# Performance work log

Hardware: AMD Instinct MI355X
Metric: run time of the kernel (lower is better)

The kernel has to match this reference:

```python
import jax, jax.numpy as jnp
import numpy as np

B, N, IN, H, E, P, L = 32, 5000, 16, 64, 2_560_000, 300, 100


def setup_inputs() -> dict:
    key = jax.random.key(0)
    ks = jax.random.split(key, 10)
    return {
        "h": jax.random.normal(ks[0], (B * N, IN), jnp.float32),
        "src": jax.random.randint(ks[1], (E,), 0, B * N, jnp.int32),
        "dst": jax.random.randint(ks[2], (E,), 0, B * N, jnp.int32),
        "pathway": jax.random.randint(ks[3], (P, L), 0, N, jnp.int32),
        "num_graphs": B,
        "W1": jax.random.normal(ks[4], (IN, H), jnp.float32) / np.float32(np.sqrt(IN)),
        "b1": jnp.zeros((H,), jnp.float32),
        "W2": jax.random.normal(ks[5], (H, H), jnp.float32) / np.float32(np.sqrt(H)),
        "b2": jnp.zeros((H,), jnp.float32),
        "w_lin1": jax.random.normal(ks[6], (2 * H, 1), jnp.float32) / np.float32(np.sqrt(2 * H)),
        "b_lin1": jnp.zeros((1,), jnp.float32),
        "W_out": jax.random.normal(ks[7], (P, 2), jnp.float32) / np.float32(np.sqrt(P)),
        "b_out": jnp.zeros((2,), jnp.float32),
    }


def reference(h, src, dst, pathway, num_graphs, W1, b1, W2, b2, w_lin1, b_lin1, W_out, b_out):
    BN = h.shape[0]
    # GINConv (eps=0, 'sum' aggregation): lin(h + sum_{j in N(i)} h_j), then relu
    agg0 = jax.ops.segment_sum(h[src], dst, num_segments=BN)
    h1 = jax.nn.relu((h + agg0) @ W1 + b1)            # [BN, H]
    agg1 = jax.ops.segment_sum(h1[src], dst, num_segments=BN)
    h2 = jax.nn.relu((h1 + agg1) @ W2 + b2)           # [BN, H]

    Hd = h2.shape[-1]
    hb = h2.reshape(num_graphs, -1, Hd)               # [B, N, H]
    Pn = pathway.shape[0]
    # Faithful to source: mean branch is the WHOLE-graph mean repeated per pathway
    mean_rep = jnp.broadcast_to(hb.mean(axis=1)[:, None, :], (num_graphs, Pn, Hd))
    # Sum-pool over each pathway's node subset
    sum_path = hb[:, pathway, :].sum(axis=2)          # [B, P, H]
    feat = jnp.concatenate([mean_rep, sum_path], axis=-1)  # [B, P, 2H]
    s = jnp.tanh(feat @ w_lin1 + b_lin1)[..., 0]      # [B, P]
    return jax.nn.softmax(s @ W_out + b_out, axis=-1)  # [B, 2]
```

## Files before the change

### kernel.cpp

```cpp
#include <hip/hip_runtime.h>
#include <hip/hip_bf16.h>
#include <math.h>

static inline size_t align256(size_t x) { return (x + 255) & ~size_t(255); }

#define SLOTS 48

__global__ __launch_bounds__(256) void place_shard(const int* __restrict__ src,
                                                   const int* __restrict__ dst,
                                                   int* __restrict__ counts,
                                                   int* __restrict__ esrc_pad, int E, int BN) {
    int s  = blockIdx.x & 7;
    int bs = blockIdx.x >> 3;
    int nb = gridDim.x >> 3;
    int lo = (int)(((long long)BN * s) >> 3);
    int hi = (int)(((long long)BN * (s + 1)) >> 3);
    for (int e = bs * 256 + threadIdx.x; e < E; e += nb * 256) {
        int d = __builtin_nontemporal_load(dst + e);
        if (d >= lo && d < hi) {
            int rank = atomicAdd(&counts[d], 1);
            if (rank < SLOTS)
                esrc_pad[(size_t)d * SLOTS + rank] = __builtin_nontemporal_load(src + e);
        }
    }
}

__global__ __launch_bounds__(256, 8) void gin1_fused(const float* __restrict__ h,
                                                     const int* __restrict__ cnts,
                                                     const int* __restrict__ esrc_pad,
                                                     const float* __restrict__ W1,
                                                     const float* __restrict__ b1,
                                                     __hip_bfloat16* __restrict__ h1, int BN) {
    __shared__ float xb[4][16];
    __shared__ int   ibuf[4][64];
    int tid = threadIdx.x;
    int lane = tid & 63, wv = tid >> 6;
    int fg = lane >> 4, ft = lane & 15;
    int gw = (int)((blockIdx.x * blockDim.x + tid) >> 6);
    int nw = (int)((gridDim.x * blockDim.x) >> 6);
    float wcol[16];
#pragma unroll
    for (int k = 0; k < 16; ++k) wcol[k] = W1[k * 64 + lane];
    float breg = b1[lane];
    for (int i = gw; i < BN; i += nw) {
        float acc = (fg == 0) ? h[(size_t)i * 16 + ft] : 0.f;
        int deg = min(cnts[i], SLOTS);
        if (lane < deg) ibuf[wv][lane] = esrc_pad[(size_t)i * SLOTS + lane];
        int jj = fg;
        for (; jj + 4 < deg; jj += 8) {
            int s0 = ibuf[wv][jj];
            int s1 = ibuf[wv][jj + 4];
            acc += h[(size_t)s0 * 16 + ft] + h[(size_t)s1 * 16 + ft];
        }
        if (jj < deg) acc += h[(size_t)ibuf[wv][jj] * 16 + ft];
        acc += __shfl_xor(acc, 16, 64);
        acc += __shfl_xor(acc, 32, 64);
        if (lane < 16) xb[wv][lane] = acc;
        float o = breg;
#pragma unroll
        for (int k4 = 0; k4 < 4; ++k4) {
            float4 xv = *(const float4*)&xb[wv][k4 * 4];
            o = fmaf(xv.x, wcol[k4 * 4 + 0], o);
            o = fmaf(xv.y, wcol[k4 * 4 + 1], o);
            o = fmaf(xv.z, wcol[k4 * 4 + 2], o);
            o = fmaf(xv.w, wcol[k4 * 4 + 3], o);
        }
        h1[(size_t)i * 64 + lane] = __float2bfloat16(fmaxf(o, 0.f));
    }
}

__global__ __launch_bounds__(256, 8) void gather64_bf16(const __hip_bfloat16* __restrict__ h1,
                                                        const int* __restrict__ cnts,
                                                        const int* __restrict__ esrc_pad,
                                                        __hip_bfloat16* __restrict__ tmp, int BN) {
    __shared__ int ibuf[4][64];
    int tid = threadIdx.x;
    int lane = tid & 63, wv = tid >> 6;
    int gw = (int)((blockIdx.x * blockDim.x + tid) >> 6);
    int nw = (int)((gridDim.x * blockDim.x) >> 6);
    const __hip_bfloat16* hl = h1 + lane;
    for (int i = gw; i < BN; i += nw) {
        float acc = __bfloat162float(hl[(size_t)i * 64]);
        int deg = min(cnts[i], SLOTS);
        if (lane < deg) ibuf[wv][lane] = esrc_pad[(size_t)i * SLOTS + lane];
        int jj = 0;
        for (; jj + 16 <= deg; jj += 16) {
            int4 ia = *(const int4*)&ibuf[wv][jj];
            int4 ib = *(const int4*)&ibuf[wv][jj + 4];
            int4 ic = *(const int4*)&ibuf[wv][jj + 8];
            int4 id = *(const int4*)&ibuf[wv][jj + 12];
            float v0 = __bfloat162float(hl[(size_t)ia.x * 64]);
            float v1 = __bfloat162float(hl[(size_t)ia.y * 64]);
            float v2 = __bfloat162float(hl[(size_t)ia.z * 64]);
            float v3 = __bfloat162float(hl[(size_t)ia.w * 64]);
            float v4 = __bfloat162float(hl[(size_t)ib.x * 64]);
            float v5 = __bfloat162float(hl[(size_t)ib.y * 64]);
            float v6 = __bfloat162float(hl[(size_t)ib.z * 64]);
            float v7 = __bfloat162float(hl[(size_t)ib.w * 64]);
            float v8 = __bfloat162float(hl[(size_t)ic.x * 64]);
            float v9 = __bfloat162float(hl[(size_t)ic.y * 64]);
            float va = __bfloat162float(hl[(size_t)ic.z * 64]);
            float vb = __bfloat162float(hl[(size_t)ic.w * 64]);
            float vc = __bfloat162float(hl[(size_t)id.x * 64]);
            float vd = __bfloat162float(hl[(size_t)id.y * 64]);
            float ve = __bfloat162float(hl[(size_t)id.z * 64]);
            float vf = __bfloat162float(hl[(size_t)id.w * 64]);
            acc += (((v0 + v1) + (v2 + v3)) + ((v4 + v5) + (v6 + v7)))
                 + (((v8 + v9) + (va + vb)) + ((vc + vd) + (ve + vf)));
        }
        for (; jj + 8 <= deg; jj += 8) {
            int4 ia = *(const int4*)&ibuf[wv][jj];
            int4 ib = *(const int4*)&ibuf[wv][jj + 4];
            float v0 = __bfloat162float(hl[(size_t)ia.x * 64]);
            float v1 = __bfloat162float(hl[(size_t)ia.y * 64]);
            float v2 = __bfloat162float(hl[(size_t)ia.z * 64]);
            float v3 = __bfloat162float(hl[(size_t)ia.w * 64]);
            float v4 = __bfloat162float(hl[(size_t)ib.x * 64]);
            float v5 = __bfloat162float(hl[(size_t)ib.y * 64]);
            float v6 = __bfloat162float(hl[(size_t)ib.z * 64]);
            float v7 = __bfloat162float(hl[(size_t)ib.w * 64]);
            acc += ((v0 + v1) + (v2 + v3)) + ((v4 + v5) + (v6 + v7));
        }
        for (; jj + 4 <= deg; jj += 4) {
            int4 ia = *(const int4*)&ibuf[wv][jj];
            float v0 = __bfloat162float(hl[(size_t)ia.x * 64]);
            float v1 = __bfloat162float(hl[(size_t)ia.y * 64]);
            float v2 = __bfloat162float(hl[(size_t)ia.z * 64]);
            float v3 = __bfloat162float(hl[(size_t)ia.w * 64]);
            acc += (v0 + v1) + (v2 + v3);
        }
        for (; jj < deg; ++jj) acc += __bfloat162float(hl[(size_t)ibuf[wv][jj] * 64]);
        tmp[(size_t)i * 64 + lane] = __float2bfloat16(acc);
    }
}

__global__ __launch_bounds__(256, 4) void lin2_qr(const __hip_bfloat16* __restrict__ tmp,
                                                  const float* __restrict__ W2,
                                                  const float* __restrict__ b2,
                                                  const float* __restrict__ wlin,
                                                  float* __restrict__ q,
                                                  float* __restrict__ r, int BN) {
    __shared__ float xbuf[4][64];
    int tid = threadIdx.x;
    int lane = tid & 63, wv = tid >> 6;
    int gw = (int)((blockIdx.x * blockDim.x + tid) >> 6);
    int nw = (int)((gridDim.x * blockDim.x) >> 6);
    float wcol[64];
#pragma unroll
    for (int k = 0; k < 64; ++k) wcol[k] = W2[k * 64 + lane];
    float breg = b2[lane];
    float wlo = wlin[lane];
    float whi = wlin[64 + lane];
    for (int i = gw; i < BN; i += nw) {
        xbuf[wv][lane] = __bfloat162float(tmp[(size_t)i * 64 + lane]);
        float outv = breg;
#pragma unroll
        for (int k4 = 0; k4 < 16; ++k4) {
            float4 xv = *(const float4*)&xbuf[wv][k4 * 4];
            outv = fmaf(xv.x, wcol[k4 * 4 + 0], outv);
            outv = fmaf(xv.y, wcol[k4 * 4 + 1], outv);
            outv = fmaf(xv.z, wcol[k4 * 4 + 2], outv);
            outv = fmaf(xv.w, wcol[k4 * 4 + 3], outv);
        }
        float h2v = fmaxf(outv, 0.f);
        float qv = h2v * whi;
        float rv = h2v * wlo;
#pragma unroll
        for (int off = 32; off >= 1; off >>= 1) {
            qv += __shfl_xor(qv, off, 64);
            rv += __shfl_xor(rv, off, 64);
        }
        if (lane == 0) {
            q[i] = qv;
            r[i] = rv;
        }
    }
}


__global__ __launch_bounds__(256) void reduce_m2(const float* __restrict__ r,
                                                 float* __restrict__ m2, int N, int bpg) {
    int b = blockIdx.x / bpg, sub = blockIdx.x % bpg;
    const float* rb = r + (size_t)b * N;
    float a = 0.f;
    for (int n = sub * 256 + threadIdx.x; n < N; n += bpg * 256) a += rb[n];
    __shared__ float red[256];
    red[threadIdx.x] = a;
    __syncthreads();
    for (int off = 128; off >= 1; off >>= 1) {
        if (threadIdx.x < off) red[threadIdx.x] += red[threadIdx.x + off];
        __syncthreads();
    }
    if (threadIdx.x == 0) unsafeAtomicAdd(&m2[b], red[0]);
}

__global__ __launch_bounds__(256) void pathway_score_wave(const float* __restrict__ q,
                                                          const int* __restrict__ pathway,
                                                          const float* __restrict__ m2,
                                                          const float* __restrict__ blin,
                                                          float* __restrict__ s,
                                                          int N, int P, int L, float invN,
                                                          int B) {
    int wid = (int)((blockIdx.x * blockDim.x + threadIdx.x) >> 6);
    int lane = threadIdx.x & 63;
    if (wid >= B * P) return;
    int b = wid / P, p = wid % P;
    const int* pw = pathway + (size_t)p * L;
    const float* qb = q + (size_t)b * N;
    float sum = 0.f;
    for (int l = lane; l < L; l += 64) sum += qb[pw[l]];
#pragma unroll
    for (int off = 32; off >= 1; off >>= 1) sum += __shfl_xor(sum, off, 64);
    if (lane == 0) s[wid] = tanhf(sum + m2[b] * invN + blin[0]);
}

__global__ __launch_bounds__(64) void out_softmax_wave(const float* __restrict__ s,
                                                       const float* __restrict__ Wout,
                                                       const float* __restrict__ bout,
                                                       float* __restrict__ out, int P) {
    int b = blockIdx.x;
    int lane = threadIdx.x;
    const float* sb = s + (size_t)b * P;
    float a0 = 0.f, a1 = 0.f;
    for (int p = lane; p < P; p += 64) {
        float sv = sb[p];
        a0 = fmaf(sv, Wout[p * 2 + 0], a0);
        a1 = fmaf(sv, Wout[p * 2 + 1], a1);
    }
#pragma unroll
    for (int off = 32; off >= 1; off >>= 1) {
        a0 += __shfl_xor(a0, off, 64);
        a1 += __shfl_xor(a1, off, 64);
    }
    if (lane == 0) {
        float l0 = a0 + bout[0], l1 = a1 + bout[1];
        float m = fmaxf(l0, l1);
        float e0 = expf(l0 - m), e1 = expf(l1 - m);
        float inv = 1.f / (e0 + e1);
        out[b * 2 + 0] = e0 * inv;
        out[b * 2 + 1] = e1 * inv;
    }
}

extern "C" void kernel_launch(void* const* d_in, const int* in_sizes, int n_in,
                              void* d_out, int out_size, void* d_ws, size_t ws_size,
                              hipStream_t stream) {
    const float* h       = (const float*)d_in[0];
    const int*   src     = (const int*)d_in[1];
    const int*   dst     = (const int*)d_in[2];
    const int*   pathway = (const int*)d_in[3];
    const float* W1      = (const float*)d_in[5];
    const float* b1      = (const float*)d_in[6];
    const float* W2      = (const float*)d_in[7];
    const float* b2      = (const float*)d_in[8];
    const float* wlin    = (const float*)d_in[9];
    const float* blin    = (const float*)d_in[10];
    const float* Wout    = (const float*)d_in[11];
    const float* bout    = (const float*)d_in[12];
    float*       out     = (float*)d_out;

    const int BN = in_sizes[0] / 16;
    const int E  = in_sizes[1];
    const int P  = in_sizes[11] / 2;
    const int L  = in_sizes[3] / P;
    const int B  = out_size / 2;
    const int N  = BN / B;

    char* ws = (char*)d_ws;
    size_t o = 0;
    __hip_bfloat16* h1  = (__hip_bfloat16*)(ws + o); o += align256((size_t)BN * 64 * 2);
    __hip_bfloat16* tmp = (__hip_bfloat16*)(ws + o); o += align256((size_t)BN * 64 * 2);
    float* qbuf     = (float*)(ws + o); o += align256((size_t)BN * 4);
    float* rbuf     = (float*)(ws + o); o += align256((size_t)BN * 4);
    float* m2       = (float*)(ws + o); o += align256((size_t)B * 4);
    float* sbuf     = (float*)(ws + o); o += align256((size_t)B * P * 4);
    int*   counts   = (int*)(ws + o);   o += align256((size_t)BN * 4);
    int*   esrc_pad = (int*)(ws + o);   o += align256((size_t)BN * SLOTS * 4);
    (void)ws_size; (void)n_in;

    hipMemsetAsync(counts, 0, (size_t)BN * 4, stream);
    hipMemsetAsync(m2, 0, (size_t)B * 4, stream);
    place_shard<<<2048, 256, 0, stream>>>(src, dst, counts, esrc_pad, E, BN);

    gin1_fused<<<4096, 256, 0, stream>>>(h, counts, esrc_pad, W1, b1, h1, BN);

    gather64_bf16<<<4096, 256, 0, stream>>>(h1, counts, esrc_pad, tmp, BN);
    lin2_qr<<<2048, 256, 0, stream>>>(tmp, W2, b2, wlin, qbuf, rbuf, BN);

    reduce_m2<<<B * 8, 256, 0, stream>>>(rbuf, m2, N, 8);
    pathway_score_wave<<<(B * P + 3) / 4, 256, 0, stream>>>(qbuf, pathway, m2, blin, sbuf,
                                                            N, P, L, 1.0f / (float)N, B);
    out_softmax_wave<<<B, 64, 0, stream>>>(sbuf, Wout, bout, out, P);
}
```

Before: 289.4 us.

## Drop destination-sharded edge placement and gather layer-1 inputs from bf16 copy

The edge bucketing kernel no longer makes each block scan every edge eight times (once per destination shard). It now processes each edge once with a global atomic, trading lower dst read traffic for less locality in the atomics and scattered writes. Separately, the input features are converted to bf16 in a new pass, so the first GIN gather reads half as many bytes per neighbour row. This adds an extra kernel launch and introduces bf16 rounding into the layer-1 aggregation.

```diff
diff --git a/kernel.cpp b/kernel.cpp
--- a/kernel.cpp
+++ b/kernel.cpp
@@ -6,26 +6,35 @@
 
 #define SLOTS 48
 
-__global__ __launch_bounds__(256) void place_shard(const int* __restrict__ src,
-                                                   const int* __restrict__ dst,
-                                                   int* __restrict__ counts,
-                                                   int* __restrict__ esrc_pad, int E, int BN) {
-    int s  = blockIdx.x & 7;
-    int bs = blockIdx.x >> 3;
-    int nb = gridDim.x >> 3;
-    int lo = (int)(((long long)BN * s) >> 3);
-    int hi = (int)(((long long)BN * (s + 1)) >> 3);
-    for (int e = bs * 256 + threadIdx.x; e < E; e += nb * 256) {
+__global__ __launch_bounds__(256) void place_pad(const int* __restrict__ src,
+                                                 const int* __restrict__ dst,
+                                                 int* __restrict__ counts,
+                                                 int* __restrict__ esrc_pad, int E) {
+    int stride = gridDim.x * 256;
+    for (int e = blockIdx.x * 256 + threadIdx.x; e < E; e += stride) {
         int d = __builtin_nontemporal_load(dst + e);
-        if (d >= lo && d < hi) {
-            int rank = atomicAdd(&counts[d], 1);
-            if (rank < SLOTS)
-                esrc_pad[(size_t)d * SLOTS + rank] = __builtin_nontemporal_load(src + e);
-        }
-    }
-}
-
-__global__ __launch_bounds__(256, 8) void gin1_fused(const float* __restrict__ h,
+        int rank = atomicAdd(&counts[d], 1);
+        if (rank < SLOTS)
+            esrc_pad[(size_t)d * SLOTS + rank] = __builtin_nontemporal_load(src + e);
+    }
+}
+
+__global__ __launch_bounds__(256) void h_to_bf16(const float4* __restrict__ hf,
+                                                 ushort4* __restrict__ hb, int n4) {
+    int stride = gridDim.x * 256;
+    for (int t = blockIdx.x * 256 + threadIdx.x; t < n4; t += stride) {
+        float4 v = hf[t];
+        union { __hip_bfloat16 b; unsigned short u; } cx, cy, cz, cw;
+        cx.b = __float2bfloat16(v.x);
+        cy.b = __float2bfloat16(v.y);
+        cz.b = __float2bfloat16(v.z);
+        cw.b = __float2bfloat16(v.w);
+        ushort4 o; o.x = cx.u; o.y = cy.u; o.z = cz.u; o.w = cw.u;
+        hb[t] = o;
+    }
+}
+
+__global__ __launch_bounds__(256, 8) void gin1_fused(const __hip_bfloat16* __restrict__ hb,
                                                      const int* __restrict__ cnts,
                                                      const int* __restrict__ esrc_pad,
                                                      const float* __restrict__ W1,
@@ -43,16 +52,17 @@
     for (int k = 0; k < 16; ++k) wcol[k] = W1[k * 64 + lane];
     float breg = b1[lane];
     for (int i = gw; i < BN; i += nw) {
-        float acc = (fg == 0) ? h[(size_t)i * 16 + ft] : 0.f;
+        float acc = (fg == 0) ? __bfloat162float(hb[(size_t)i * 16 + ft]) : 0.f;
         int deg = min(cnts[i], SLOTS);
         if (lane < deg) ibuf[wv][lane] = esrc_pad[(size_t)i * SLOTS + lane];
         int jj = fg;
         for (; jj + 4 < deg; jj += 8) {
             int s0 = ibuf[wv][jj];
             int s1 = ibuf[wv][jj + 4];
-            acc += h[(size_t)s0 * 16 + ft] + h[(size_t)s1 * 16 + ft];
-        }
-        if (jj < deg) acc += h[(size_t)ibuf[wv][jj] * 16 + ft];
+            acc += __bfloat162float(hb[(size_t)s0 * 16 + ft])
+                 + __bfloat162float(hb[(size_t)s1 * 16 + ft]);
+        }
+        if (jj < deg) acc += __bfloat162float(hb[(size_t)ibuf[wv][jj] * 16 + ft]);
         acc += __shfl_xor(acc, 16, 64);
         acc += __shfl_xor(acc, 32, 64);
         if (lane < 16) xb[wv][lane] = acc;
@@ -270,6 +280,7 @@
     size_t o = 0;
     __hip_bfloat16* h1  = (__hip_bfloat16*)(ws + o); o += align256((size_t)BN * 64 * 2);
     __hip_bfloat16* tmp = (__hip_bfloat16*)(ws + o); o += align256((size_t)BN * 64 * 2);
+    __hip_bfloat16* hb  = (__hip_bfloat16*)(ws + o); o += align256((size_t)BN * 16 * 2);
     float* qbuf     = (float*)(ws + o); o += align256((size_t)BN * 4);
     float* rbuf     = (float*)(ws + o); o += align256((size_t)BN * 4);
     float* m2       = (float*)(ws + o); o += align256((size_t)B * 4);
@@ -280,9 +291,10 @@
 
     hipMemsetAsync(counts, 0, (size_t)BN * 4, stream);
     hipMemsetAsync(m2, 0, (size_t)B * 4, stream);
-    place_shard<<<2048, 256, 0, stream>>>(src, dst, counts, esrc_pad, E, BN);
-
-    gin1_fused<<<4096, 256, 0, stream>>>(h, counts, esrc_pad, W1, b1, h1, BN);
+    place_pad<<<2048, 256, 0, stream>>>(src, dst, counts, esrc_pad, E);
+    h_to_bf16<<<1024, 256, 0, stream>>>((const float4*)h, (ushort4*)hb, BN * 4);
+
+    gin1_fused<<<4096, 256, 0, stream>>>(hb, counts, esrc_pad, W1, b1, h1, BN);
 
     gather64_bf16<<<4096, 256, 0, stream>>>(h1, counts, esrc_pad, tmp, BN);
     lin2_qr<<<2048, 256, 0, stream>>>(tmp, W2, b2, wlin, qbuf, rbuf, BN);
```

Result: slower. 310.3 us (+7.2%).
